# Optimization experiments

Hardware: AMD Instinct MI355X
Metric: run time of the kernel (lower is better)

The kernel has to match this reference:

```python
import jax, jax.numpy as jnp
import numpy as np

VIN, VOUT, E, H = 32000, 32000, 1024, 1024
TS, TT, B = 50, 48, 64


def _lstm_scan(x, m, Wih, Whh, bih, bhh):
    """Masked (packed-sequence-equivalent) LSTM. x:(T,B,E), m:(T,B) bool valid."""
    Bn, Hn = x.shape[1], Whh.shape[1]

    def step(carry, tm):
        h, c = carry
        xt, mt = tm
        gates = xt @ Wih.T + bih + h @ Whh.T + bhh
        i, f, g, o = jnp.split(gates, 4, axis=-1)  # torch gate order i,f,g,o
        c_new = jax.nn.sigmoid(f) * c + jax.nn.sigmoid(i) * jnp.tanh(g)
        h_new = jax.nn.sigmoid(o) * jnp.tanh(c_new)
        mt_ = mt[:, None]
        return (jnp.where(mt_, h_new, h), jnp.where(mt_, c_new, c)), jnp.where(mt_, h_new, 0.0)

    init = (jnp.zeros((Bn, Hn), x.dtype), jnp.zeros((Bn, Hn), x.dtype))
    (h, c), outs = jax.lax.scan(step, init, (x, m))
    return outs, h, c


def setup_inputs() -> dict:
    key = jax.random.key(0)
    ks = jax.random.split(key, 32)
    s = 0.02
    src = jax.random.randint(ks[0], (TS, B), 0, VIN)
    src_len = jnp.sort(jax.random.randint(ks[1], (B,), TS // 2, TS + 1))[::-1]
    src_len = src_len.at[0].set(TS)  # pad_packed pads to max length in batch
    trg = jax.random.randint(ks[2], (TT, B), 0, VOUT)
    p = lambda k, shp: jax.random.normal(k, shp, jnp.float32) * s
    return {
        "src": src, "src_len": src_len, "trg": trg,
        "enc_emb": p(ks[3], (VIN, E)),
        "Wih_f": p(ks[4], (4 * H, E)), "Whh_f": p(ks[5], (4 * H, H)),
        "bih_f": p(ks[6], (4 * H,)), "bhh_f": p(ks[7], (4 * H,)),
        "Wih_b": p(ks[8], (4 * H, E)), "Whh_b": p(ks[9], (4 * H, H)),
        "bih_b": p(ks[10], (4 * H,)), "bhh_b": p(ks[11], (4 * H,)),
        "Wfch": p(ks[12], (H, 2 * H)), "bfch": p(ks[13], (H,)),
        "Wfcc": p(ks[14], (H, 2 * H)), "bfcc": p(ks[15], (H,)),
        "dec_emb": p(ks[16], (VOUT, H)),
        "Wih_d": p(ks[17], (4 * H, 2 * H)), "Whh_d": p(ks[18], (4 * H, H)),
        "bih_d": p(ks[19], (4 * H,)), "bhh_d": p(ks[20], (4 * H,)),
        "Wattn": p(ks[21], (H, 2 * H)), "battn": p(ks[22], (H,)),
        "Wcomb": p(ks[23], (H, 3 * H)), "bcomb": p(ks[24], (H,)),
        "Wout": p(ks[25], (VOUT, H)), "bout": p(ks[26], (VOUT,)),
    }


def reference(src, src_len, trg, enc_emb, Wih_f, Whh_f, bih_f, bhh_f,
              Wih_b, Whh_b, bih_b, bhh_b, Wfch, bfch, Wfcc, bfcc, dec_emb,
              Wih_d, Whh_d, bih_d, bhh_d, Wattn, battn, Wcomb, bcomb, Wout, bout):
    T, Bn = src.shape
    emb = enc_emb[src]                                      # (T,B,E)
    m = jnp.arange(T)[:, None] < src_len[None, :]           # (T,B) valid
    outs_f, hf, cf = _lstm_scan(emb, m, Wih_f, Whh_f, bih_f, bhh_f)
    outs_b, hb, cb = _lstm_scan(emb[::-1], m[::-1], Wih_b, Whh_b, bih_b, bhh_b)
    outs_b = outs_b[::-1]
    enc_outputs = jnp.concatenate([outs_f, outs_b], -1).transpose(1, 0, 2)  # (B,T,2H)
    hidden = jnp.concatenate([hf, hb], -1) @ Wfch.T + bfch  # (B,H)
    cell = jnp.concatenate([cf, cb], -1) @ Wfcc.T + bfcc
    mask_pad = ~m.T                                          # (B,T) True at pads

    attn_proj = jnp.einsum('btd,hd->bth', enc_outputs, Wattn) + battn  # (B,T,H)
    dec_emb_seq = dec_emb[trg]                               # (TT,B,H), dropout=eval

    def dstep(carry, emb_t):
        h, c, dout = carry
        x = jnp.concatenate([emb_t, dout], -1)               # (B, H+H)
        gates = x @ Wih_d.T + bih_d + h @ Whh_d.T + bhh_d
        i, f, g, o = jnp.split(gates, 4, axis=-1)
        c_new = jax.nn.sigmoid(f) * c + jax.nn.sigmoid(i) * jnp.tanh(g)
        h_new = jax.nn.sigmoid(o) * jnp.tanh(c_new)
        scores = jnp.einsum('bth,bh->bt', attn_proj, h_new)
        scores = jnp.where(mask_pad, -jnp.inf, scores)
        w = jax.nn.softmax(scores, -1)
        ctx = jnp.einsum('bt,btd->bd', w, enc_outputs)       # (B,2H)
        dout_new = jnp.concatenate([ctx, h_new], -1) @ Wcomb.T + bcomb
        logits = jax.nn.relu(dout_new) @ Wout.T + bout       # (B,VOUT)
        return (h_new, c_new, dout_new), logits

    init = (hidden, cell, jnp.zeros_like(hidden))
    _, logits = jax.lax.scan(dstep, init, dec_emb_seq[:-1])  # (TT-1,B,V)
    return logits.transpose(1, 2, 0)                         # (B,V,TT-1)
```

## Files before the change

### kernel.cpp

```cpp
#include <hip/hip_runtime.h>
#include <hip/hip_bf16.h>
#include <math.h>


typedef __attribute__((ext_vector_type(8))) short short8;
typedef __attribute__((ext_vector_type(4))) float floatx4;
typedef unsigned short u16;

#define DEV static __device__ __forceinline__

DEV float bf2f(u16 u){ union{unsigned int i; float f;} v; v.i = ((unsigned int)u)<<16; return v.f; }
DEV u16 f2bf(float f){
  union{float f; unsigned int i;} v; v.f = f;
  unsigned int i = v.i;
  return (u16)((i + 0x7fffu + ((i>>16)&1u)) >> 16);
}
DEV float sigm(float x){ return 1.f/(1.f+expf(-x)); }

__global__ __launch_bounds__(256) void cvt2d(const float* __restrict__ src, long sld,
                                             u16* __restrict__ dst, long dld, long cols)
{
  long r = blockIdx.x;
  long c = ((long)blockIdx.y*256 + threadIdx.x)*4;
  if (c >= cols) return;
  const float4 v = *(const float4*)(src + r*sld + c);
  u16* d = dst + r*dld + c;
  d[0]=f2bf(v.x); d[1]=f2bf(v.y); d[2]=f2bf(v.z); d[3]=f2bf(v.w);
}

DEV void split_store(const float4 v, u16* d, u16* e){
  u16 h0=f2bf(v.x), h1=f2bf(v.y), h2=f2bf(v.z), h3=f2bf(v.w);
  d[0]=h0; d[1]=h1; d[2]=h2; d[3]=h3;
  e[0]=f2bf(v.x-bf2f(h0)); e[1]=f2bf(v.y-bf2f(h1));
  e[2]=f2bf(v.z-bf2f(h2)); e[3]=f2bf(v.w-bf2f(h3));
}

__global__ __launch_bounds__(256) void cvtA(
    const float* s0, const float* s1, const float* s2, const float* s3,
    u16* h0, u16* h1, u16* h2, u16* h3,
    u16* l0, u16* l1, u16* l2, u16* l3)
{
  const float* s; u16* h; u16* l;
  switch (blockIdx.z){
    case 0: s=s0; h=h0; l=l0; break;
    case 1: s=s1; h=h1; l=l1; break;
    case 2: s=s2; h=h2; l=l2; break;
    default: s=s3; h=h3; l=l3; break;
  }
  long r = blockIdx.x; long c = (long)threadIdx.x*4;
  split_store(*(const float4*)(s + r*1024 + c), h + r*1024 + c, l + r*1024 + c);
}

__global__ __launch_bounds__(256) void cvtB(
    const float* s0, long sld0, const float* s1, long sld1,
    const float* s2, long sld2, const float* s3, long sld3,
    u16* h0, u16* h1, u16* h2, u16* h3,
    u16* l0, u16* l1, u16* l2, u16* l3)
{
  const float* s; u16* h; u16* l; long sld;
  switch (blockIdx.z){
    case 0: s=s0; h=h0; l=l0; sld=sld0; break;
    case 1: s=s1; h=h1; l=l1; sld=sld1; break;
    case 2: s=s2; h=h2; l=l2; sld=sld2; break;
    default: s=s3; h=h3; l=l3; sld=sld3; break;
  }
  long r = blockIdx.x;
  long c = ((long)blockIdx.y*256 + threadIdx.x)*4;
  split_store(*(const float4*)(s + r*sld + c), h + r*2048 + c, l + r*2048 + c);
}

__global__ __launch_bounds__(256) void cvtC(
    const float* s0, long sld0, u16* h0, u16* l0, long dld0,
    const float* s1, long sld1, u16* h1, u16* l1, long dld1,
    const float* s2, long sld2, u16* h2, u16* l2, long dld2)
{
  const float* s; u16* h; u16* l; long sld, dld;
  switch (blockIdx.z){
    case 0: s=s0; h=h0; l=l0; sld=sld0; dld=dld0; break;
    case 1: s=s1; h=h1; l=l1; sld=sld1; dld=dld1; break;
    default: s=s2; h=h2; l=l2; sld=sld2; dld=dld2; break;
  }
  long r = blockIdx.x; long c = (long)threadIdx.x*4;
  split_store(*(const float4*)(s + r*sld + c), h + r*dld + c, l + r*dld + c);
}

__global__ __launch_bounds__(256) void cvt_cell_split(const float* __restrict__ c_all,
                                                      u16* __restrict__ hi, u16* __restrict__ lo)
{
  int b = blockIdx.x, tid = threadIdx.x;
  for (int k = 0; k < 8; k++){
    int u = tid + k*256;
    int dir = u >> 10, uu = u & 1023;
    float v = c_all[dir*65536 + b*1024 + uu];
    u16 h = f2bf(v);
    hi[b*2048 + u] = h;
    lo[b*2048 + u] = f2bf(v - bf2f(h));
  }
}

__global__ __launch_bounds__(256) void bias_combine(
    const float* a1,const float* a2,float* o1,
    const float* b1,const float* b2,float* o2,
    const float* c1,const float* c2,float* o3,
    const float* battn, float* o4)
{
  int i = blockIdx.x*256 + threadIdx.x;
  if (i < 4096){ o1[i]=a1[i]+a2[i]; o2[i]=b1[i]+b2[i]; o3[i]=c1[i]+c2[i]; }
  if (i < 2048) o4[i] = (i < 1024) ? battn[i] : 0.f;
}

__global__ __launch_bounds__(256) void zero_u32(unsigned int* p, int n){
  int i = blockIdx.x*256 + threadIdx.x;
  if (i < n) p[i] = 0;
}

__global__ __launch_bounds__(256) void gather_embed_split(const int* __restrict__ idx,
                                                          const float* __restrict__ tab,
                                                          u16* __restrict__ hi, u16* __restrict__ lo)
{
  int r = blockIdx.x, tid = threadIdx.x;
  int tok = idx[r];
  float4 v = ((const float4*)(tab + (long)tok*1024))[tid];
  split_store(v, hi + (long)r*1024 + tid*4, lo + (long)r*1024 + tid*4);
}

template<int AS, int BS>
__global__ __launch_bounds__(256) void gemm128(
    const u16* __restrict__ Ahi, const u16* __restrict__ Alo, int lda,
    const u16* __restrict__ Bhi, const u16* __restrict__ Blo, int ldb,
    int M, int N, int K,
    const float* __restrict__ bias,
    float* __restrict__ Cf, int ldc)
{
  __shared__ u16 Ash[128][36];
  __shared__ u16 Bsh[128][36];
  __shared__ u16 Asl[AS?128:1][36];
  __shared__ u16 Bsl[BS?128:1][36];
  const int tid = threadIdx.x;
  const int lane = tid & 63;
  const int w = tid >> 6, wm = w >> 1, wn = w & 1;
  const int m0 = blockIdx.x * 128;
  const int n0 = blockIdx.y * 128;

  floatx4 acc[4][4];
  #pragma unroll
  for (int i=0;i<4;i++)
    #pragma unroll
    for (int j=0;j<4;j++) acc[i][j] = (floatx4)0.f;

  const int seg = tid & 3;
  const int rowh = tid >> 2;
  const int nk = K >> 5;
  for (int kk = 0; kk < nk; kk++) {
    int kbase = kk*32 + seg*8;
    #pragma unroll
    for (int p=0;p<2;p++){
      int r = rowh + p*64;
      bool okA = (m0 + r < M);
      int4 va = okA ? *(const int4*)(Ahi + (long)(m0+r)*lda + kbase) : make_int4(0,0,0,0);
      *(int4*)&Ash[r][seg*8] = va;
      if (AS){
        int4 vl = okA ? *(const int4*)(Alo + (long)(m0+r)*lda + kbase) : make_int4(0,0,0,0);
        *(int4*)&Asl[r][seg*8] = vl;
      }
      *(int4*)&Bsh[r][seg*8] = *(const int4*)(Bhi + (long)(n0+r)*ldb + kbase);
      if (BS)
        *(int4*)&Bsl[r][seg*8] = *(const int4*)(Blo + (long)(n0+r)*ldb + kbase);
    }
    __syncthreads();
    short8 ah[4], bh[4], al[4], bl[4];
    #pragma unroll
    for (int i=0;i<4;i++){
      ah[i] = *(const short8*)&Ash[wm*64 + i*16 + (lane&15)][(lane>>4)*8];
      if (AS) al[i] = *(const short8*)&Asl[wm*64 + i*16 + (lane&15)][(lane>>4)*8];
    }
    #pragma unroll
    for (int j=0;j<4;j++){
      bh[j] = *(const short8*)&Bsh[wn*64 + j*16 + (lane&15)][(lane>>4)*8];
      if (BS) bl[j] = *(const short8*)&Bsl[wn*64 + j*16 + (lane&15)][(lane>>4)*8];
    }
    #pragma unroll
    for (int i=0;i<4;i++)
      #pragma unroll
      for (int j=0;j<4;j++){
        acc[i][j] = __builtin_amdgcn_mfma_f32_16x16x32_bf16(ah[i], bh[j], acc[i][j], 0,0,0);
        if (AS) acc[i][j] = __builtin_amdgcn_mfma_f32_16x16x32_bf16(al[i], bh[j], acc[i][j], 0,0,0);
        if (BS) acc[i][j] = __builtin_amdgcn_mfma_f32_16x16x32_bf16(ah[i], bl[j], acc[i][j], 0,0,0);
      }
    __syncthreads();
  }
  const int rb0 = (lane>>4)*4, cf = lane & 15;
  #pragma unroll
  for (int i=0;i<4;i++){
    #pragma unroll
    for (int j=0;j<4;j++){
      int n = n0 + wn*64 + j*16 + cf;
      #pragma unroll
      for (int r=0;r<4;r++){
        int m = m0 + wm*64 + i*16 + rb0 + r;
        if (m >= M) continue;
        Cf[(long)m*ldc + n] = acc[i][j][r] + (bias ? bias[n] : 0.f);
      }
    }
  }
}

template<int MODE>
__global__ __launch_bounds__(256) void gemm64(
    const u16* __restrict__ Ahi, const u16* __restrict__ Alo, int lda,
    const u16* __restrict__ Bhi, const u16* __restrict__ Blo, int ldb,
    int K, const float* __restrict__ bias,
    float* __restrict__ outF,
    u16* __restrict__ o1hi, u16* __restrict__ o1lo)
{
  __shared__ u16 Ash[64][36], Asl[64][36];
  __shared__ u16 Bsh[64][36], Bsl[64][36];
  const int tid = threadIdx.x, lane = tid&63, w = tid>>6;
  const int n0 = blockIdx.x * 64;
  floatx4 acc[4];
  #pragma unroll
  for (int i=0;i<4;i++) acc[i]=(floatx4)0.f;
  const int seg = tid&3, row = tid>>2;
  const int nk = K>>5;
  for (int kk=0; kk<nk; kk++){
    int kbase = kk*32 + seg*8;
    *(int4*)&Ash[row][seg*8] = *(const int4*)(Ahi + (long)row*lda + kbase);
    *(int4*)&Asl[row][seg*8] = *(const int4*)(Alo + (long)row*lda + kbase);
    *(int4*)&Bsh[row][seg*8] = *(const int4*)(Bhi + (long)(n0+row)*ldb + kbase);
    *(int4*)&Bsl[row][seg*8] = *(const int4*)(Blo + (long)(n0+row)*ldb + kbase);
    __syncthreads();
    short8 bh = *(const short8*)&Bsh[w*16 + (lane&15)][(lane>>4)*8];
    short8 bl = *(const short8*)&Bsl[w*16 + (lane&15)][(lane>>4)*8];
    #pragma unroll
    for (int i=0;i<4;i++){
      short8 ah = *(const short8*)&Ash[i*16 + (lane&15)][(lane>>4)*8];
      short8 al = *(const short8*)&Asl[i*16 + (lane&15)][(lane>>4)*8];
      acc[i] = __builtin_amdgcn_mfma_f32_16x16x32_bf16(ah, bh, acc[i], 0,0,0);
      acc[i] = __builtin_amdgcn_mfma_f32_16x16x32_bf16(al, bh, acc[i], 0,0,0);
      acc[i] = __builtin_amdgcn_mfma_f32_16x16x32_bf16(ah, bl, acc[i], 0,0,0);
    }
    __syncthreads();
  }
  const int rb0 = (lane>>4)*4, cf = lane&15;
  int n = n0 + w*16 + cf;
  #pragma unroll
  for (int i=0;i<4;i++){
    #pragma unroll
    for (int r=0;r<4;r++){
      int m = i*16 + rb0 + r;
      float v = acc[i][r] + bias[n];
      if (MODE == 0){
        u16 h = f2bf(v), l = f2bf(v - bf2f(h));
        o1hi[m*2048 + n] = h; o1lo[m*2048 + n] = l;
      } else {
        outF[m*1024 + n] = v;
      }
    }
  }
}

__global__ __launch_bounds__(256) void enc_step(
    int s,
    const u16* __restrict__ hin_hi, const u16* __restrict__ hin_lo,
    u16* __restrict__ hout_hi, u16* __restrict__ hout_lo,
    float* __restrict__ c_all,
    const u16* __restrict__ Whhf_hi, const u16* __restrict__ Whhf_lo,
    const u16* __restrict__ Whhb_hi, const u16* __restrict__ Whhb_lo,
    const float* __restrict__ Gfb,
    const float* __restrict__ bias_f, const float* __restrict__ bias_b,
    const int* __restrict__ src_len,
    u16* __restrict__ eo_hi, u16* __restrict__ eo_lo)
{
  __shared__ u16 Ah[32][1032], Al[32][1032];
  __shared__ float gl[4][32][17];
  const int tid = threadIdx.x, lane = tid&63, w = tid>>6;
  const int b0  = (blockIdx.x >> 7) * 32;
  const int dir = (blockIdx.x >> 6) & 1;
  const int u0  = (blockIdx.x & 63) * 16;
  const u16* Whh_hi = dir ? Whhb_hi : Whhf_hi;
  const u16* Whh_lo = dir ? Whhb_lo : Whhf_lo;
  const float* bias = dir ? bias_b : bias_f;
  const int trow = dir ? (49 - s) : s;

  {
    int row = tid>>3, c0 = (tid&7)*8;
    const u16* sh = hin_hi + dir*1024 + (b0+row)*2048;
    const u16* sl = hin_lo + dir*1024 + (b0+row)*2048;
    #pragma unroll
    for (int j=0;j<16;j++){
      int c = c0 + j*64;
      *(int4*)&Ah[row][c] = *(const int4*)(sh + c);
      *(int4*)&Al[row][c] = *(const int4*)(sl + c);
    }
  }
  __syncthreads();

  const int rowb = w*1024 + u0 + (lane&15);
  const int cseg = (lane>>4)*8;
  const u16* bhp = Whh_hi + (long)rowb*1024 + cseg;
  const u16* blp = Whh_lo + (long)rowb*1024 + cseg;
  floatx4 acc0 = (floatx4)0.f, acc1 = (floatx4)0.f;
  #pragma unroll 4
  for (int kk=0; kk<32; kk++){
    int kbase = kk*32;
    short8 bh = *(const short8*)(bhp + kbase);
    short8 bl = *(const short8*)(blp + kbase);
    short8 ah0 = *(const short8*)&Ah[lane&15][kbase + cseg];
    short8 al0 = *(const short8*)&Al[lane&15][kbase + cseg];
    short8 ah1 = *(const short8*)&Ah[16 + (lane&15)][kbase + cseg];
    short8 al1 = *(const short8*)&Al[16 + (lane&15)][kbase + cseg];
    acc0 = __builtin_amdgcn_mfma_f32_16x16x32_bf16(ah0, bh, acc0, 0,0,0);
    acc0 = __builtin_amdgcn_mfma_f32_16x16x32_bf16(al0, bh, acc0, 0,0,0);
    acc0 = __builtin_amdgcn_mfma_f32_16x16x32_bf16(ah0, bl, acc0, 0,0,0);
    acc1 = __builtin_amdgcn_mfma_f32_16x16x32_bf16(ah1, bh, acc1, 0,0,0);
    acc1 = __builtin_amdgcn_mfma_f32_16x16x32_bf16(al1, bh, acc1, 0,0,0);
    acc1 = __builtin_amdgcn_mfma_f32_16x16x32_bf16(ah1, bl, acc1, 0,0,0);
  }
  __syncthreads();
  const int rb0 = (lane>>4)*4, cf = lane&15;
  #pragma unroll
  for (int r=0;r<4;r++){
    gl[w][rb0 + r][cf]      = acc0[r];
    gl[w][16 + rb0 + r][cf] = acc1[r];
  }
  __syncthreads();
  for (int k=0;k<2;k++){
    int idx = tid + k*256;
    int bl_ = idx >> 4, u = idx & 15;
    int b = b0 + bl_, uu = u0 + u;
    long grow = (long)(trow*64 + b)*8192 + dir*4096;
    float gi = gl[0][bl_][u] + Gfb[grow +        uu] + bias[uu];
    float gf = gl[1][bl_][u] + Gfb[grow + 1024 + uu] + bias[1024+uu];
    float gg2 = gl[2][bl_][u] + Gfb[grow + 2048 + uu] + bias[2048+uu];
    float go = gl[3][bl_][u] + Gfb[grow + 3072 + uu] + bias[3072+uu];
    float c_old = c_all[dir*65536 + b*1024 + uu];
    float c_new = sigm(gf)*c_old + sigm(gi)*tanhf(gg2);
    float h_new = sigm(go)*tanhf(c_new);
    bool valid = trow < src_len[b];
    if (valid) c_all[dir*65536 + b*1024 + uu] = c_new;
    u16 hh = f2bf(h_new);
    u16 hl = f2bf(h_new - bf2f(hh));
    int hidx = b*2048 + dir*1024 + uu;
    hout_hi[hidx] = valid ? hh : hin_hi[hidx];
    hout_lo[hidx] = valid ? hl : hin_lo[hidx];
    long eidx = (long)(b*50 + trow)*2048 + dir*1024 + uu;
    eo_hi[eidx] = valid ? hh : (u16)0;
    eo_lo[eidx] = valid ? hl : (u16)0;
  }
}

__global__ __launch_bounds__(256) void dec_gates(
    int t,
    const u16* __restrict__ ain_hi, const u16* __restrict__ ain_lo,
    u16* __restrict__ aout_hi, u16* __restrict__ aout_lo,
    float* __restrict__ c_dec,
    const u16* __restrict__ Wcat_hi, const u16* __restrict__ Wcat_lo,
    const float* __restrict__ Gd,
    const float* __restrict__ bias_d,
    float* __restrict__ hf32)
{
  __shared__ u16 Ah[16][2056], Al[16][2056];
  __shared__ float gl[4][16][17];
  const int tid=threadIdx.x, lane=tid&63, w=tid>>6;
  const int b0 = (blockIdx.x >> 6) * 16;
  const int u0 = (blockIdx.x & 63) * 16;

  {
    int row = tid>>4, c0 = (tid&15)*8;
    const u16* sh = ain_hi + (b0+row)*2048;
    const u16* sl = ain_lo + (b0+row)*2048;
    #pragma unroll
    for (int j=0;j<16;j++){
      int c = c0 + j*128;
      *(int4*)&Ah[row][c] = *(const int4*)(sh + c);
      *(int4*)&Al[row][c] = *(const int4*)(sl + c);
    }
  }
  __syncthreads();

  const int rowb = w*1024 + u0 + (lane&15);
  const int cseg = (lane>>4)*8;
  const u16* bhp = Wcat_hi + (long)rowb*2048 + cseg;
  const u16* blp = Wcat_lo + (long)rowb*2048 + cseg;
  floatx4 acc = (floatx4)0.f;
  #pragma unroll 4
  for (int kk=0; kk<64; kk++){
    int kbase = kk*32;
    short8 bh = *(const short8*)(bhp + kbase);
    short8 bl = *(const short8*)(blp + kbase);
    short8 ah = *(const short8*)&Ah[lane&15][kbase + cseg];
    short8 al = *(const short8*)&Al[lane&15][kbase + cseg];
    acc = __builtin_amdgcn_mfma_f32_16x16x32_bf16(ah,bh,acc,0,0,0);
    acc = __builtin_amdgcn_mfma_f32_16x16x32_bf16(al,bh,acc,0,0,0);
    acc = __builtin_amdgcn_mfma_f32_16x16x32_bf16(ah,bl,acc,0,0,0);
  }
  __syncthreads();
  const int rb0=(lane>>4)*4, cf=lane&15;
  #pragma unroll
  for(int r=0;r<4;r++) gl[w][rb0+r][cf] = acc[r];
  __syncthreads();
  {
    int bl_ = tid>>4, u = tid&15;
    int b = b0 + bl_, uu = u0 + u;
    long grow = (long)(t*64 + b)*4096;
    float gi = gl[0][bl_][u] + Gd[grow +        uu] + bias_d[uu];
    float gf = gl[1][bl_][u] + Gd[grow + 1024 + uu] + bias_d[1024+uu];
    float gg2 = gl[2][bl_][u] + Gd[grow + 2048 + uu] + bias_d[2048+uu];
    float go = gl[3][bl_][u] + Gd[grow + 3072 + uu] + bias_d[3072+uu];
    float c_old = c_dec[b*1024+uu];
    float c_new = sigm(gf)*c_old + sigm(gi)*tanhf(gg2);
    float h_new = sigm(go)*tanhf(c_new);
    c_dec[b*1024+uu] = c_new;
    u16 hh = f2bf(h_new);
    u16 hl = f2bf(h_new - bf2f(hh));
    aout_hi[b*2048 + uu] = hh;  aout_lo[b*2048 + uu] = hl;
    hf32[b*1024 + uu] = h_new;
  }
}

__global__ __launch_bounds__(256) void attn_w(
    const float* __restrict__ APf,
    const float* __restrict__ hf32,
    const int* __restrict__ src_len,
    float* __restrict__ wout)
{
  __shared__ float h_sh[1024];
  __shared__ float sc_sh[50];
  const int tid = threadIdx.x, lane = tid&63, w = tid>>6;
  const int b = blockIdx.x;
  for (int i = tid; i < 1024; i += 256) h_sh[i] = hf32[b*1024 + i];
  __syncthreads();
  for (int tp = w; tp < 50; tp += 4){
    const float* ap = APf + (long)(b*50+tp)*2048;
    float p = 0.f;
    #pragma unroll
    for (int i=0;i<16;i++){ int d = lane + i*64; p += ap[d]*h_sh[d]; }
    #pragma unroll
    for (int off=32; off>0; off>>=1) p += __shfl_down(p, off);
    if (lane==0) sc_sh[tp] = p;
  }
  __syncthreads();
  if (w == 0){
    int len = src_len[b];
    float s = (lane < 50 && lane < len) ? sc_sh[lane] : -3.4e38f;
    float mx = s;
    #pragma unroll
    for (int off=32; off>0; off>>=1) mx = fmaxf(mx, __shfl_xor(mx, off));
    float p = (lane < 50 && lane < len) ? expf(s - mx) : 0.f;
    float sum = p;
    #pragma unroll
    for (int off=32; off>0; off>>=1) sum += __shfl_xor(sum, off);
    if (lane < 50) wout[b*50 + lane] = p / sum;
  }
}

__global__ __launch_bounds__(256) void dout_step(
    int t,
    const u16* __restrict__ h_hi, const u16* __restrict__ h_lo,
    const u16* __restrict__ Wch_h, const u16* __restrict__ Wch_l,
    const float* __restrict__ APf,
    const float* __restrict__ wout,
    const float* __restrict__ bcomb,
    u16* __restrict__ ac_hi, u16* __restrict__ ac_lo,
    u16* __restrict__ dall_h)
{
  __shared__ u16 Ash[4][16][36], Asl[4][16][36];
  __shared__ u16 Bsh[4][16][36], Bsl[4][16][36];
  __shared__ float gl[4][16][17];
  const int tid=threadIdx.x, lane=tid&63, w=tid>>6;
  const int b0 = ((blockIdx.x >> 6) & 3) * 16;
  const int n0 = (blockIdx.x & 63) * 16;
  floatx4 acc = (floatx4)0.f;
  const int r = lane&15, sg = lane>>4;
  for (int kk=0; kk<8; kk++){
    int kb = w*256 + kk*32 + sg*8;
    *(int4*)&Ash[w][r][sg*8] = *(const int4*)(h_hi + (b0+r)*2048 + kb);
    *(int4*)&Asl[w][r][sg*8] = *(const int4*)(h_lo + (b0+r)*2048 + kb);
    *(int4*)&Bsh[w][r][sg*8] = *(const int4*)(Wch_h + (long)(n0+r)*1024 + kb);
    *(int4*)&Bsl[w][r][sg*8] = *(const int4*)(Wch_l + (long)(n0+r)*1024 + kb);
    __syncthreads();
    short8 ah = *(const short8*)&Ash[w][lane&15][(lane>>4)*8];
    short8 al = *(const short8*)&Asl[w][lane&15][(lane>>4)*8];
    short8 bh = *(const short8*)&Bsh[w][lane&15][(lane>>4)*8];
    short8 bl = *(const short8*)&Bsl[w][lane&15][(lane>>4)*8];
    acc = __builtin_amdgcn_mfma_f32_16x16x32_bf16(ah,bh,acc,0,0,0);
    acc = __builtin_amdgcn_mfma_f32_16x16x32_bf16(al,bh,acc,0,0,0);
    acc = __builtin_amdgcn_mfma_f32_16x16x32_bf16(ah,bl,acc,0,0,0);
    __syncthreads();
  }
  const int rb0=(lane>>4)*4, cf=lane&15;
  #pragma unroll
  for(int rr=0;rr<4;rr++) gl[w][rb0+rr][cf] = acc[rr];
  __syncthreads();
  {
    int bl_ = tid>>4, nl = tid&15;
    int b = b0 + bl_, nn = n0 + nl;
    float v = gl[0][bl_][nl]+gl[1][bl_][nl]+gl[2][bl_][nl]+gl[3][bl_][nl] + bcomb[nn];
    const float* wp = wout + b*50;
    const float* Pp = APf + (long)(b*50)*2048 + 1024 + nn;
    for (int tp=0; tp<50; tp++) v += wp[tp] * Pp[(long)tp*2048];
    u16 h = f2bf(v), l = f2bf(v - bf2f(h));
    ac_hi[b*2048 + 1024 + nn] = h;  ac_lo[b*2048 + 1024 + nn] = l;
    float rv = v > 0.f ? v : 0.f;
    dall_h[(long)(b*47 + t)*1024 + nn] = f2bf(rv);
  }
}

__global__ __launch_bounds__(256) void logits_gemm(
    const u16* __restrict__ Wout_bf,
    const u16* __restrict__ dall_h,
    const float* __restrict__ bout,
    float* __restrict__ out)
{
  const int x = blockIdx.x;
  const int y = blockIdx.y;
  const int cnt = (x < 5) ? 16 : 15;
  if (y >= cnt*64) return;
  const int vt = ((x < 5) ? x*16 : 80 + (x-5)*15) + (y >> 6);
  const int b  = y & 63;
  const int v0 = vt * 256;

  __shared__ u16 Wsh[256][36];
  __shared__ u16 Dh[48][36];
  const int tid = threadIdx.x, lane = tid&63, w = tid>>6;
  floatx4 acc[4][3];
  #pragma unroll
  for (int i=0;i<4;i++)
    #pragma unroll
    for (int j=0;j<3;j++) acc[i][j]=(floatx4)0.f;
  const int lrow = tid>>1, lseg = tid&1;
  for (int kk=0; kk<32; kk++){
    int kb = kk*32;
    #pragma unroll
    for (int p=0;p<2;p++){
      int row = lrow + p*128;
      const u16* src = Wout_bf + (long)(v0+row)*1024 + kb + lseg*16;
      *(int4*)&Wsh[row][lseg*16]     = *(const int4*)(src);
      *(int4*)&Wsh[row][lseg*16 + 8] = *(const int4*)(src + 8);
    }
    if (tid < 96){
      int row = tid>>1, sg = tid&1;
      long a = (long)(b*47+row)*1024 + kb + sg*16;
      *(int4*)&Dh[row][sg*16]     = *(const int4*)(dall_h + a);
      *(int4*)&Dh[row][sg*16 + 8] = *(const int4*)(dall_h + a + 8);
    }
    __syncthreads();
    short8 av[4];
    #pragma unroll
    for (int i=0;i<4;i++)
      av[i] = *(const short8*)&Wsh[w*64 + i*16 + (lane&15)][(lane>>4)*8];
    #pragma unroll
    for (int j=0;j<3;j++){
      short8 bh = *(const short8*)&Dh[j*16 + (lane&15)][(lane>>4)*8];
      #pragma unroll
      for (int i=0;i<4;i++)
        acc[i][j] = __builtin_amdgcn_mfma_f32_16x16x32_bf16(av[i], bh, acc[i][j], 0,0,0);
    }
    __syncthreads();
  }
  const int rb0=(lane>>4)*4, cf=lane&15;
  #pragma unroll
  for (int i=0;i<4;i++){
    #pragma unroll
    for (int j=0;j<3;j++){
      int tt = j*16 + cf;
      if (tt >= 47) continue;
      #pragma unroll
      for (int r=0;r<4;r++){
        int v = v0 + w*64 + i*16 + rb0 + r;
        out[(long)b*1504000 + (long)v*47 + tt] = acc[i][j][r] + bout[v];
      }
    }
  }
}

extern "C" void kernel_launch(void* const* d_in, const int* in_sizes, int n_in,
                              void* d_out, int out_size, void* d_ws, size_t ws_size,
                              hipStream_t stream)
{
  (void)in_sizes; (void)n_in; (void)out_size; (void)ws_size;
  const int*   src     = (const int*)d_in[0];
  const int*   src_len = (const int*)d_in[1];
  const int*   trg     = (const int*)d_in[2];
  const float* enc_emb = (const float*)d_in[3];
  const float* Wih_f   = (const float*)d_in[4];
  const float* Whh_f   = (const float*)d_in[5];
  const float* bih_f   = (const float*)d_in[6];
  const float* bhh_f   = (const float*)d_in[7];
  const float* Wih_b   = (const float*)d_in[8];
  const float* Whh_b   = (const float*)d_in[9];
  const float* bih_b   = (const float*)d_in[10];
  const float* bhh_b   = (const float*)d_in[11];
  const float* Wfch    = (const float*)d_in[12];
  const float* bfch    = (const float*)d_in[13];
  const float* Wfcc    = (const float*)d_in[14];
  const float* bfcc    = (const float*)d_in[15];
  const float* dec_emb = (const float*)d_in[16];
  const float* Wih_d   = (const float*)d_in[17];
  const float* Whh_d   = (const float*)d_in[18];
  const float* bih_d   = (const float*)d_in[19];
  const float* bhh_d   = (const float*)d_in[20];
  const float* Wattn   = (const float*)d_in[21];
  const float* battn   = (const float*)d_in[22];
  const float* Wcomb   = (const float*)d_in[23];
  const float* bcomb   = (const float*)d_in[24];
  const float* Wout    = (const float*)d_in[25];
  const float* bout    = (const float*)d_in[26];
  float* out = (float*)d_out;

  size_t off = 0;
  auto alloc = [&](size_t bytes)->void*{
    void* p = (char*)d_ws + off; off += (bytes + 255) & ~(size_t)255; return p; };

  u16* Wenc_h = (u16*)alloc((size_t)8192*1024*2);  u16* Wenc_l = (u16*)alloc((size_t)8192*1024*2);
  u16* Whhf_h = (u16*)alloc((size_t)4096*1024*2);  u16* Whhf_l = (u16*)alloc((size_t)4096*1024*2);
  u16* Whhb_h = (u16*)alloc((size_t)4096*1024*2);  u16* Whhb_l = (u16*)alloc((size_t)4096*1024*2);
  u16* WihdA_h= (u16*)alloc((size_t)4096*1024*2);  u16* WihdA_l= (u16*)alloc((size_t)4096*1024*2);
  u16* Wcat_h = (u16*)alloc((size_t)4096*2048*2);  u16* Wcat_l = (u16*)alloc((size_t)4096*2048*2);
  u16* Wfch_h = (u16*)alloc((size_t)1024*2048*2);  u16* Wfch_l = (u16*)alloc((size_t)1024*2048*2);
  u16* Wfcc_h = (u16*)alloc((size_t)1024*2048*2);  u16* Wfcc_l = (u16*)alloc((size_t)1024*2048*2);
  u16* Wap_h  = (u16*)alloc((size_t)2048*2048*2);  u16* Wap_l  = (u16*)alloc((size_t)2048*2048*2);
  u16* Wch_h  = (u16*)alloc((size_t)1024*1024*2);  u16* Wch_l  = (u16*)alloc((size_t)1024*1024*2);
  u16* Wout_bf =(u16*)alloc((size_t)32000*1024*2);
  u16* embx_h = (u16*)alloc((size_t)3200*1024*2);  u16* embx_l = (u16*)alloc((size_t)3200*1024*2);
  u16* dembx_h= (u16*)alloc((size_t)3008*1024*2);  u16* dembx_l= (u16*)alloc((size_t)3008*1024*2);
  float* Gfb  = (float*)alloc((size_t)3200*8192*4);
  float* Gd   = (float*)alloc((size_t)3008*4096*4);
  u16* eo_h  = (u16*)alloc((size_t)3200*2048*2);
  u16* eo_l  = (u16*)alloc((size_t)3200*2048*2);
  u16* h0_h  = (u16*)alloc((size_t)64*2048*2);  u16* h0_l  = (u16*)alloc((size_t)64*2048*2);
  u16* h1_h  = (u16*)alloc((size_t)64*2048*2);  u16* h1_l  = (u16*)alloc((size_t)64*2048*2);
  u16* cfin_h= (u16*)alloc((size_t)64*2048*2);  u16* cfin_l= (u16*)alloc((size_t)64*2048*2);
  u16* ac0_h = (u16*)alloc((size_t)64*2048*2);  u16* ac0_l = (u16*)alloc((size_t)64*2048*2);
  u16* ac1_h = (u16*)alloc((size_t)64*2048*2);  u16* ac1_l = (u16*)alloc((size_t)64*2048*2);
  u16* dall_h= (u16*)alloc((size_t)3009*1024*2);
  float* APf   = (float*)alloc((size_t)3200*2048*4);
  float* c_enc = (float*)alloc((size_t)2*64*1024*4);
  float* c_dec = (float*)alloc((size_t)64*1024*4);
  float* hf32  = (float*)alloc((size_t)64*1024*4);
  float* wout  = (float*)alloc((size_t)64*50*4);
  float* bias_f = (float*)alloc(4096*4);
  float* bias_b = (float*)alloc(4096*4);
  float* bias_d = (float*)alloc(4096*4);
  float* bias_ap= (float*)alloc(2048*4);

  cvtA<<<dim3(4096,1,4),256,0,stream>>>(Wih_f, Wih_b, Whh_f, Whh_b,
                                        Wenc_h, Wenc_h + (size_t)4096*1024, Whhf_h, Whhb_h,
                                        Wenc_l, Wenc_l + (size_t)4096*1024, Whhf_l, Whhb_l);
  cvtB<<<dim3(1024,2,4),256,0,stream>>>(Wfch, 2048, Wfcc, 2048, Wattn, 2048, Wcomb, 3072,
                                        Wfch_h, Wfcc_h, Wap_h, Wap_h + (size_t)1024*2048,
                                        Wfch_l, Wfcc_l, Wap_l, Wap_l + (size_t)1024*2048);
  cvtC<<<dim3(4096,1,3),256,0,stream>>>(Wih_d, 2048, WihdA_h, WihdA_l, 1024,
                                        Whh_d, 1024, Wcat_h, Wcat_l, 2048,
                                        Wih_d + 1024, 2048, Wcat_h + 1024, Wcat_l + 1024, 2048);
  cvtC<<<dim3(1024,1,1),256,0,stream>>>(Wcomb + 2048, 3072, Wch_h, Wch_l, 1024,
                                        Wcomb + 2048, 3072, Wch_h, Wch_l, 1024,
                                        Wcomb + 2048, 3072, Wch_h, Wch_l, 1024);
  cvt2d<<<dim3(32000,1),256,0,stream>>>(Wout, 1024, Wout_bf, 1024, 1024);
  bias_combine<<<16,256,0,stream>>>(bih_f,bhh_f,bias_f, bih_b,bhh_b,bias_b, bih_d,bhh_d,bias_d, battn,bias_ap);

  gather_embed_split<<<3200,256,0,stream>>>(src, enc_emb, embx_h, embx_l);
  gather_embed_split<<<3008,256,0,stream>>>(trg, dec_emb, dembx_h, dembx_l);

  zero_u32<<<256,256,0,stream>>>((unsigned int*)h0_h, 65536);
  zero_u32<<<256,256,0,stream>>>((unsigned int*)h0_l, 65536);
  zero_u32<<<256,256,0,stream>>>((unsigned int*)ac0_h, 65536);
  zero_u32<<<256,256,0,stream>>>((unsigned int*)ac0_l, 65536);
  zero_u32<<<512,256,0,stream>>>((unsigned int*)c_enc, 131072);

  gemm128<1,1><<<dim3(25,64),256,0,stream>>>(embx_h, embx_l, 1024, Wenc_h, Wenc_l, 1024, 3200, 8192, 1024, nullptr, Gfb, 8192);
  gemm128<1,1><<<dim3(24,32),256,0,stream>>>(dembx_h, dembx_l, 1024, WihdA_h, WihdA_l, 1024, 3008, 4096, 1024, nullptr, Gd, 4096);

  u16* hh_[2] = {h0_h, h1_h};
  u16* hl_[2] = {h0_l, h1_l};
  for (int s=0; s<50; s++)
    enc_step<<<256,256,0,stream>>>(s, hh_[s&1], hl_[s&1], hh_[(s+1)&1], hl_[(s+1)&1], c_enc,
                                   Whhf_h, Whhf_l, Whhb_h, Whhb_l, Gfb, bias_f, bias_b, src_len, eo_h, eo_l);

  cvt_cell_split<<<64,256,0,stream>>>(c_enc, cfin_h, cfin_l);

  gemm128<1,1><<<dim3(25,16),256,0,stream>>>(eo_h, eo_l, 2048, Wap_h, Wap_l, 2048, 3200, 2048, 2048, bias_ap, APf, 2048);

  gemm64<0><<<16,256,0,stream>>>(h0_h, h0_l, 2048, Wfch_h, Wfch_l, 2048, 2048, bfch, nullptr, ac0_h, ac0_l);
  gemm64<1><<<16,256,0,stream>>>(cfin_h, cfin_l, 2048, Wfcc_h, Wfcc_l, 2048, 2048, bfcc, c_dec, nullptr, nullptr);

  u16* ah_[2] = {ac0_h, ac1_h};
  u16* al_[2] = {ac0_l, ac1_l};
  for (int t=0; t<47; t++){
    int cur = t&1, nxt = (t+1)&1;
    dec_gates<<<256,256,0,stream>>>(t, ah_[cur], al_[cur], ah_[nxt], al_[nxt], c_dec,
                                    Wcat_h, Wcat_l, Gd, bias_d, hf32);
    attn_w<<<64,256,0,stream>>>(APf, hf32, src_len, wout);
    dout_step<<<256,256,0,stream>>>(t, ah_[nxt], al_[nxt], Wch_h, Wch_l, APf, wout, bcomb,
                                    ah_[nxt], al_[nxt], dall_h);
  }

  logits_gemm<<<dim3(8,1024),256,0,stream>>>(Wout_bf, dall_h, bout, out);
}
```

Before: 4.550 ms.

## Load MFMA operands directly from global in recurrent steps; two batches per logits block

In the encoder step, decoder gate and combine kernels, the shared-memory staging of the activation and weight operands is removed, along with the barriers around it. MFMA fragments are now read straight from global memory, so no block has to wait on a full tile copy before computing, and the LDS footprint drops. The logits GEMM now handles two batch rows per block, reusing each staged Wout tile twice and halving the grid and the weight reloads. The cost is more redundant global/L2 reads of the activation rows across waves, and more accumulator registers in the logits kernel, which may lower occupancy.

After: 5.342 ms. 1.17x slower.

```diff
diff --git a/kernel.cpp b/kernel.cpp
--- a/kernel.cpp
+++ b/kernel.cpp
@@ -271,7 +271,6 @@
     const int* __restrict__ src_len,
     u16* __restrict__ eo_hi, u16* __restrict__ eo_lo)
 {
-  __shared__ u16 Ah[32][1032], Al[32][1032];
   __shared__ float gl[4][32][17];
   const int tid = threadIdx.x, lane = tid&63, w = tid>>6;
   const int b0  = (blockIdx.x >> 7) * 32;
@@ -282,33 +281,26 @@
   const float* bias = dir ? bias_b : bias_f;
   const int trow = dir ? (49 - s) : s;
 
-  {
-    int row = tid>>3, c0 = (tid&7)*8;
-    const u16* sh = hin_hi + dir*1024 + (b0+row)*2048;
-    const u16* sl = hin_lo + dir*1024 + (b0+row)*2048;
-    #pragma unroll
-    for (int j=0;j<16;j++){
-      int c = c0 + j*64;
-      *(int4*)&Ah[row][c] = *(const int4*)(sh + c);
-      *(int4*)&Al[row][c] = *(const int4*)(sl + c);
-    }
-  }
-  __syncthreads();
-
-  const int rowb = w*1024 + u0 + (lane&15);
+  const int lane15 = lane & 15;
   const int cseg = (lane>>4)*8;
+  const u16* a0h = hin_hi + dir*1024 + (long)(b0+lane15)*2048 + cseg;
+  const u16* a0l = hin_lo + dir*1024 + (long)(b0+lane15)*2048 + cseg;
+  const u16* a1h = a0h + 16*2048;
+  const u16* a1l = a0l + 16*2048;
+  const int rowb = w*1024 + u0 + lane15;
   const u16* bhp = Whh_hi + (long)rowb*1024 + cseg;
   const u16* blp = Whh_lo + (long)rowb*1024 + cseg;
+
   floatx4 acc0 = (floatx4)0.f, acc1 = (floatx4)0.f;
   #pragma unroll 4
   for (int kk=0; kk<32; kk++){
     int kbase = kk*32;
     short8 bh = *(const short8*)(bhp + kbase);
     short8 bl = *(const short8*)(blp + kbase);
-    short8 ah0 = *(const short8*)&Ah[lane&15][kbase + cseg];
-    short8 al0 = *(const short8*)&Al[lane&15][kbase + cseg];
-    short8 ah1 = *(const short8*)&Ah[16 + (lane&15)][kbase + cseg];
-    short8 al1 = *(const short8*)&Al[16 + (lane&15)][kbase + cseg];
+    short8 ah0 = *(const short8*)(a0h + kbase);
+    short8 al0 = *(const short8*)(a0l + kbase);
+    short8 ah1 = *(const short8*)(a1h + kbase);
+    short8 al1 = *(const short8*)(a1l + kbase);
     acc0 = __builtin_amdgcn_mfma_f32_16x16x32_bf16(ah0, bh, acc0, 0,0,0);
     acc0 = __builtin_amdgcn_mfma_f32_16x16x32_bf16(al0, bh, acc0, 0,0,0);
     acc0 = __builtin_amdgcn_mfma_f32_16x16x32_bf16(ah0, bl, acc0, 0,0,0);
@@ -316,12 +308,11 @@
     acc1 = __builtin_amdgcn_mfma_f32_16x16x32_bf16(al1, bh, acc1, 0,0,0);
     acc1 = __builtin_amdgcn_mfma_f32_16x16x32_bf16(ah1, bl, acc1, 0,0,0);
   }
-  __syncthreads();
-  const int rb0 = (lane>>4)*4, cf = lane&15;
+  const int rb0 = (lane>>4)*4;
   #pragma unroll
   for (int r=0;r<4;r++){
-    gl[w][rb0 + r][cf]      = acc0[r];
-    gl[w][16 + rb0 + r][cf] = acc1[r];
+    gl[w][rb0 + r][lane15]      = acc0[r];
+    gl[w][16 + rb0 + r][lane15] = acc1[r];
   }
   __syncthreads();
   for (int k=0;k<2;k++){
@@ -359,45 +350,34 @@
     const float* __restrict__ bias_d,
     float* __restrict__ hf32)
 {
-  __shared__ u16 Ah[16][2056], Al[16][2056];
   __shared__ float gl[4][16][17];
   const int tid=threadIdx.x, lane=tid&63, w=tid>>6;
   const int b0 = (blockIdx.x >> 6) * 16;
   const int u0 = (blockIdx.x & 63) * 16;
 
-  {
-    int row = tid>>4, c0 = (tid&15)*8;
-    const u16* sh = ain_hi + (b0+row)*2048;
-    const u16* sl = ain_lo + (b0+row)*2048;
-    #pragma unroll
-    for (int j=0;j<16;j++){
-      int c = c0 + j*128;
-      *(int4*)&Ah[row][c] = *(const int4*)(sh + c);
-      *(int4*)&Al[row][c] = *(const int4*)(sl + c);
-    }
-  }
-  __syncthreads();
-
-  const int rowb = w*1024 + u0 + (lane&15);
+  const int lane15 = lane & 15;
   const int cseg = (lane>>4)*8;
+  const u16* aph = ain_hi + (long)(b0+lane15)*2048 + cseg;
+  const u16* apl = ain_lo + (long)(b0+lane15)*2048 + cseg;
+  const int rowb = w*1024 + u0 + lane15;
   const u16* bhp = Wcat_hi + (long)rowb*2048 + cseg;
   const u16* blp = Wcat_lo + (long)rowb*2048 + cseg;
+
   floatx4 acc = (floatx4)0.f;
   #pragma unroll 4
   for (int kk=0; kk<64; kk++){
     int kbase = kk*32;
     short8 bh = *(const short8*)(bhp + kbase);
     short8 bl = *(const short8*)(blp + kbase);
-    short8 ah = *(const short8*)&Ah[lane&15][kbase + cseg];
-    short8 al = *(const short8*)&Al[lane&15][kbase + cseg];
+    short8 ah = *(const short8*)(aph + kbase);
+    short8 al = *(const short8*)(apl + kbase);
     acc = __builtin_amdgcn_mfma_f32_16x16x32_bf16(ah,bh,acc,0,0,0);
     acc = __builtin_amdgcn_mfma_f32_16x16x32_bf16(al,bh,acc,0,0,0);
     acc = __builtin_amdgcn_mfma_f32_16x16x32_bf16(ah,bl,acc,0,0,0);
   }
-  __syncthreads();
-  const int rb0=(lane>>4)*4, cf=lane&15;
-  #pragma unroll
-  for(int r=0;r<4;r++) gl[w][rb0+r][cf] = acc[r];
+  const int rb0=(lane>>4)*4;
+  #pragma unroll
+  for(int r=0;r<4;r++) gl[w][rb0+r][lane15] = acc[r];
   __syncthreads();
   {
     int bl_ = tid>>4, u = tid&15;
@@ -464,33 +444,33 @@
     u16* __restrict__ ac_hi, u16* __restrict__ ac_lo,
     u16* __restrict__ dall_h)
 {
-  __shared__ u16 Ash[4][16][36], Asl[4][16][36];
-  __shared__ u16 Bsh[4][16][36], Bsl[4][16][36];
   __shared__ float gl[4][16][17];
   const int tid=threadIdx.x, lane=tid&63, w=tid>>6;
   const int b0 = ((blockIdx.x >> 6) & 3) * 16;
   const int n0 = (blockIdx.x & 63) * 16;
+
+  const int lane15 = lane & 15;
+  const int cseg = (lane>>4)*8;
+  const u16* aph = h_hi + (long)(b0+lane15)*2048 + w*256 + cseg;
+  const u16* apl = h_lo + (long)(b0+lane15)*2048 + w*256 + cseg;
+  const u16* bph = Wch_h + (long)(n0+lane15)*1024 + w*256 + cseg;
+  const u16* bpl = Wch_l + (long)(n0+lane15)*1024 + w*256 + cseg;
+
   floatx4 acc = (floatx4)0.f;
-  const int r = lane&15, sg = lane>>4;
+  #pragma unroll
   for (int kk=0; kk<8; kk++){
-    int kb = w*256 + kk*32 + sg*8;
-    *(int4*)&Ash[w][r][sg*8] = *(const int4*)(h_hi + (b0+r)*2048 + kb);
-    *(int4*)&Asl[w][r][sg*8] = *(const int4*)(h_lo + (b0+r)*2048 + kb);
-    *(int4*)&Bsh[w][r][sg*8] = *(const int4*)(Wch_h + (long)(n0+r)*1024 + kb);
-    *(int4*)&Bsl[w][r][sg*8] = *(const int4*)(Wch_l + (long)(n0+r)*1024 + kb);
-    __syncthreads();
-    short8 ah = *(const short8*)&Ash[w][lane&15][(lane>>4)*8];
-    short8 al = *(const short8*)&Asl[w][lane&15][(lane>>4)*8];
-    short8 bh = *(const short8*)&Bsh[w][lane&15][(lane>>4)*8];
-    short8 bl = *(const short8*)&Bsl[w][lane&15][(lane>>4)*8];
+    int kbase = kk*32;
+    short8 ah = *(const short8*)(aph + kbase);
+    short8 al = *(const short8*)(apl + kbase);
+    short8 bh = *(const short8*)(bph + kbase);
+    short8 bl = *(const short8*)(bpl + kbase);
     acc = __builtin_amdgcn_mfma_f32_16x16x32_bf16(ah,bh,acc,0,0,0);
     acc = __builtin_amdgcn_mfma_f32_16x16x32_bf16(al,bh,acc,0,0,0);
     acc = __builtin_amdgcn_mfma_f32_16x16x32_bf16(ah,bl,acc,0,0,0);
-    __syncthreads();
-  }
-  const int rb0=(lane>>4)*4, cf=lane&15;
-  #pragma unroll
-  for(int rr=0;rr<4;rr++) gl[w][rb0+rr][cf] = acc[rr];
+  }
+  const int rb0=(lane>>4)*4;
+  #pragma unroll
+  for(int rr=0;rr<4;rr++) gl[w][rb0+rr][lane15] = acc[rr];
   __syncthreads();
   {
     int bl_ = tid>>4, nl = tid&15;
@@ -515,19 +495,21 @@
   const int x = blockIdx.x;
   const int y = blockIdx.y;
   const int cnt = (x < 5) ? 16 : 15;
-  if (y >= cnt*64) return;
-  const int vt = ((x < 5) ? x*16 : 80 + (x-5)*15) + (y >> 6);
-  const int b  = y & 63;
+  if (y >= cnt*32) return;
+  const int vt = ((x < 5) ? x*16 : 80 + (x-5)*15) + (y >> 5);
+  const int b0 = (y & 31)*2;
   const int v0 = vt * 256;
 
   __shared__ u16 Wsh[256][36];
-  __shared__ u16 Dh[48][36];
+  __shared__ u16 Dh[2][48][36];
   const int tid = threadIdx.x, lane = tid&63, w = tid>>6;
-  floatx4 acc[4][3];
-  #pragma unroll
-  for (int i=0;i<4;i++)
-    #pragma unroll
-    for (int j=0;j<3;j++) acc[i][j]=(floatx4)0.f;
+  floatx4 acc[2][4][3];
+  #pragma unroll
+  for (int bb=0;bb<2;bb++)
+    #pragma unroll
+    for (int i=0;i<4;i++)
+      #pragma unroll
+      for (int j=0;j<3;j++) acc[bb][i][j]=(floatx4)0.f;
   const int lrow = tid>>1, lseg = tid&1;
   for (int kk=0; kk<32; kk++){
     int kb = kk*32;
@@ -538,11 +520,12 @@
       *(int4*)&Wsh[row][lseg*16]     = *(const int4*)(src);
       *(int4*)&Wsh[row][lseg*16 + 8] = *(const int4*)(src + 8);
     }
-    if (tid < 96){
-      int row = tid>>1, sg = tid&1;
-      long a = (long)(b*47+row)*1024 + kb + sg*16;
-      *(int4*)&Dh[row][sg*16]     = *(const int4*)(dall_h + a);
-      *(int4*)&Dh[row][sg*16 + 8] = *(const int4*)(dall_h + a + 8);
+    if (tid < 192){
+      int bb = tid/96, t2 = tid - bb*96;
+      int row = t2>>1, sg = t2&1;
+      long a = (long)((b0+bb)*47+row)*1024 + kb + sg*16;
+      *(int4*)&Dh[bb][row][sg*16]     = *(const int4*)(dall_h + a);
+      *(int4*)&Dh[bb][row][sg*16 + 8] = *(const int4*)(dall_h + a + 8);
     }
     __syncthreads();
     short8 av[4];
@@ -551,24 +534,30 @@
       av[i] = *(const short8*)&Wsh[w*64 + i*16 + (lane&15)][(lane>>4)*8];
     #pragma unroll
     for (int j=0;j<3;j++){
-      short8 bh = *(const short8*)&Dh[j*16 + (lane&15)][(lane>>4)*8];
       #pragma unroll
-      for (int i=0;i<4;i++)
-        acc[i][j] = __builtin_amdgcn_mfma_f32_16x16x32_bf16(av[i], bh, acc[i][j], 0,0,0);
+      for (int bb=0;bb<2;bb++){
+        short8 bh = *(const short8*)&Dh[bb][j*16 + (lane&15)][(lane>>4)*8];
+        #pragma unroll
+        for (int i=0;i<4;i++)
+          acc[bb][i][j] = __builtin_amdgcn_mfma_f32_16x16x32_bf16(av[i], bh, acc[bb][i][j], 0,0,0);
+      }
     }
     __syncthreads();
   }
   const int rb0=(lane>>4)*4, cf=lane&15;
   #pragma unroll
-  for (int i=0;i<4;i++){
-    #pragma unroll
-    for (int j=0;j<3;j++){
-      int tt = j*16 + cf;
-      if (tt >= 47) continue;
+  for (int bb=0;bb<2;bb++){
+    #pragma unroll
+    for (int i=0;i<4;i++){
       #pragma unroll
-      for (int r=0;r<4;r++){
-        int v = v0 + w*64 + i*16 + rb0 + r;
-        out[(long)b*1504000 + (long)v*47 + tt] = acc[i][j][r] + bout[v];
+      for (int j=0;j<3;j++){
+        int tt = j*16 + cf;
+        if (tt >= 47) continue;
+        #pragma unroll
+        for (int r=0;r<4;r++){
+          int v = v0 + w*64 + i*16 + rb0 + r;
+          out[(long)(b0+bb)*1504000 + (long)v*47 + tt] = acc[bb][i][j][r] + bout[v];
+        }
       }
     }
   }
@@ -695,5 +684,5 @@
                                     ah_[nxt], al_[nxt], dall_h);
   }
 
-  logits_gemm<<<dim3(8,1024),256,0,stream>>>(Wout_bf, dall_h, bout, out);
-}
+  logits_gemm<<<dim3(8,512),256,0,stream>>>(Wout_bf, dall_h, bout, out);
+}
```
